# Kernel tuning notes

Hardware: AMD Instinct MI355X
Metric: run time of the kernel (lower is better)

## Reference

```python
import jax, jax.numpy as jnp
import numpy as np

IN_F = 3
HID = 256
N_HIDDEN = 4  # number of hidden SineLayers after the first
OUT_F = 3
OMEGA_0 = 30.0
OMEGA_H = 30.0
N_PTS = 262144


def _uniform(key, shape, bound):
    return jax.random.uniform(key, shape, jnp.float32, -bound, bound)


def setup_inputs() -> dict:
    key = jax.random.key(0)
    ks = jax.random.split(key, 8)
    # coordinates in [-1, 1]
    x = jax.random.uniform(ks[0], (N_PTS, IN_F), jnp.float32, -1.0, 1.0)
    # first layer: W ~ U(-1/n, 1/n)
    w_first = _uniform(ks[1], (HID, IN_F), 1.0 / IN_F)
    b_first = _uniform(ks[2], (HID,), 1.0 / np.sqrt(IN_F))
    # hidden layers: W ~ U(-sqrt(6/n)/omega, sqrt(6/n)/omega), stacked for scan
    hb = np.sqrt(6.0 / HID) / OMEGA_H
    w_hidden = _uniform(ks[3], (N_HIDDEN, HID, HID), hb)
    b_hidden = _uniform(ks[4], (N_HIDDEN, HID), 1.0 / np.sqrt(HID))
    # final linear: same SIREN bound with omega=30
    fb = np.sqrt(6.0 / HID) / 30.0
    w_final = _uniform(ks[5], (OUT_F, HID), fb)
    b_final = _uniform(ks[6], (OUT_F,), 1.0 / np.sqrt(HID))
    return {
        "x": x,
        "w_first": w_first,
        "b_first": b_first,
        "w_hidden": w_hidden,
        "b_hidden": b_hidden,
        "w_final": w_final,
        "b_final": b_final,
    }


def reference(x, w_first, b_first, w_hidden, b_hidden, w_final, b_final):
    # first sine layer: sin(omega_0 * (x W^T + b))
    h = jnp.sin(OMEGA_0 * (x @ w_first.T + b_first))

    # hidden sine layers via scan over stacked [L, HID, HID] weights
    def step(h, wb):
        w, b = wb
        return jnp.sin(OMEGA_H * (h @ w.T + b)), None

    h, _ = jax.lax.scan(step, h, (w_hidden, b_hidden))
    # final linear (no activation: final_activation=None)
    return h @ w_final.T + b_final
```

## Files before the change

### kernel.cpp

```cpp
#include <hip/hip_runtime.h>


typedef _Float16 hf8 __attribute__((ext_vector_type(8)));
typedef _Float16 hf4 __attribute__((ext_vector_type(4)));
typedef float floatx4 __attribute__((ext_vector_type(4)));
typedef unsigned short u16;

#define HID 256
#define NHID 4
#define BM 64
#define THREADS 512
#define NP (BM/16)
#define C_REV 4.774648292756860f
#define WH_ELEMS (NHID*HID*HID)
#define WS_HALVES (WH_ELEMS + 3*HID)

__device__ __forceinline__ float sin_rev(float r){
  float rr = r - rintf(r);
  float s;
  asm("v_sin_f32 %0, %1" : "=v"(s) : "v"(rr));
  return s;
}
__device__ __forceinline__ hf8 ld8h_f32(const float* f){
  const floatx4 a = *(const floatx4*)f;
  const floatx4 b = *(const floatx4*)(f + 4);
  hf8 o;
#pragma unroll
  for (int e = 0; e < 4; ++e){ o[e] = (_Float16)a[e]; o[4+e] = (_Float16)b[e]; }
  return o;
}
__device__ __forceinline__ int hoff(int r, int c){
  return r*HID + (c ^ ((r & 7) << 3));
}

__global__ void prep_kernel(const float* __restrict__ wh,
                            const float* __restrict__ wfin,
                            _Float16* __restrict__ ws){
  const int i = blockIdx.x*256 + threadIdx.x;
  if (i < WH_ELEMS)            ws[i] = (_Float16)wh[i];
  else if (i < WS_HALVES)      ws[i] = (_Float16)wfin[i - WH_ELEMS];
}

template<bool WS>
__global__ __launch_bounds__(THREADS, 4) void siren_kernel(
    const float* __restrict__ x, const float* __restrict__ w_first,
    const float* __restrict__ b_first, const float* __restrict__ w_hidden,
    const float* __restrict__ b_hidden, const float* __restrict__ w_final,
    const float* __restrict__ b_final, const _Float16* __restrict__ wsh,
    float* __restrict__ out)
{
  __shared__ __align__(16) _Float16 hbuf[2][BM*HID];
  __shared__ __align__(16) float    wf[HID*4];
  __shared__ __align__(16) _Float16 wfin[3*HID];

  const int tid = threadIdx.x;
  const int blk = blockIdx.x;

  if (tid < HID){
    wf[tid*4+0] = w_first[tid*3+0] * C_REV;
    wf[tid*4+1] = w_first[tid*3+1] * C_REV;
    wf[tid*4+2] = w_first[tid*3+2] * C_REV;
    wf[tid*4+3] = b_first[tid]     * C_REV;
  } else {
    const int i0 = (tid - HID) * 3;
#pragma unroll
    for (int j = 0; j < 3; ++j){
      const int i = i0 + j;
      if (i < 3*HID) wfin[i] = WS ? wsh[WH_ELEMS + i] : (_Float16)w_final[i];
    }
  }
  __syncthreads();

  {
    const int row = tid & (BM-1);
    const int cb  = (tid >> 6) * 32;
    const int gr  = blk*BM + row;
    const float x0 = x[gr*3+0];
    const float x1 = x[gr*3+1];
    const float x2 = x[gr*3+2];
#pragma unroll
    for (int g = 0; g < 4; ++g){
      hf8 hv;
#pragma unroll
      for (int e = 0; e < 8; ++e){
        const int j = cb + g*8 + e;
        const floatx4 w = *(const floatx4*)(&wf[j*4]);
        float r = w[3];
        r = fmaf(x0, w[0], r);
        r = fmaf(x1, w[1], r);
        r = fmaf(x2, w[2], r);
        hv[e] = (_Float16)sin_rev(r);
      }
      *(hf8*)(&hbuf[0][hoff(row, cb + g*8)]) = hv;
    }
  }
  __syncthreads();

  const int wv  = tid >> 6;
  const int l   = tid & 63;
  const int l15 = l & 15;
  const int l4  = l >> 4;

  const _Float16* rb = &hbuf[0][0];
  _Float16*       wb = &hbuf[1][0];
  for (int L = 0; L < NHID; ++L){
    hf8   wfr[2][8];
    float bC[2][4];
#pragma unroll
    for (int m2 = 0; m2 < 2; ++m2){
      const int jrow  = wv*32 + m2*16 + l15;
      const int wbase = L*HID*HID + jrow*HID + l4*8;
#pragma unroll
      for (int k = 0; k < 8; ++k){
        if (WS) wfr[m2][k] = *(const hf8*)(wsh + wbase + k*32);
        else    wfr[m2][k] = ld8h_f32(w_hidden + wbase + k*32);
      }
      const int j0 = wv*32 + m2*16 + l4*4;
#pragma unroll
      for (int g = 0; g < 4; ++g)
        bC[m2][g] = b_hidden[L*HID + j0 + g] * C_REV;
    }

#pragma unroll
    for (int np = 0; np < NP; ++np){
      const int r = np*16 + l15;
      hf8 bh[8];
#pragma unroll
      for (int k = 0; k < 8; ++k)
        bh[k] = *(const hf8*)(rb + hoff(r, k*32 + l4*8));
      floatx4 acc0 = {0.f,0.f,0.f,0.f};
      floatx4 acc1 = {0.f,0.f,0.f,0.f};
#pragma unroll
      for (int k = 0; k < 8; ++k){
        acc0 = __builtin_amdgcn_mfma_f32_16x16x32_f16(wfr[0][k], bh[k], acc0, 0, 0, 0);
        acc1 = __builtin_amdgcn_mfma_f32_16x16x32_f16(wfr[1][k], bh[k], acc1, 0, 0, 0);
      }
#pragma unroll
      for (int m2 = 0; m2 < 2; ++m2){
        const floatx4 z = m2 ? acc1 : acc0;
        hf4 hv;
#pragma unroll
        for (int g = 0; g < 4; ++g)
          hv[g] = (_Float16)sin_rev(fmaf(z[g], C_REV, bC[m2][g]));
        const int jb = wv*32 + m2*16 + l4*4;
        *(hf4*)(wb + hoff(r, jb)) = hv;
      }
    }
    _Float16* t = (_Float16*)rb; rb = wb; wb = t;
    __syncthreads();
  }

  {
    const int row = tid >> 3;
    const int q   = tid & 7;
    float s0 = 0.f, s1 = 0.f, s2 = 0.f;
#pragma unroll
    for (int i = 0; i < 4; ++i){
      const int c = q*32 + i*8;
      const hf8 hv = *(const hf8*)(rb + hoff(row, c));
      const hf8 w0 = *(const hf8*)(&wfin[0*HID + c]);
      const hf8 w1 = *(const hf8*)(&wfin[1*HID + c]);
      const hf8 w2 = *(const hf8*)(&wfin[2*HID + c]);
#pragma unroll
      for (int e = 0; e < 8; ++e){
        const float h = (float)hv[e];
        s0 = fmaf(h, (float)w0[e], s0);
        s1 = fmaf(h, (float)w1[e], s1);
        s2 = fmaf(h, (float)w2[e], s2);
      }
    }
    s0 += __shfl_xor(s0, 1); s0 += __shfl_xor(s0, 2); s0 += __shfl_xor(s0, 4);
    s1 += __shfl_xor(s1, 1); s1 += __shfl_xor(s1, 2); s1 += __shfl_xor(s1, 4);
    s2 += __shfl_xor(s2, 1); s2 += __shfl_xor(s2, 2); s2 += __shfl_xor(s2, 4);
    if (q == 0){
      const int gr = blk*BM + row;
      out[gr*3+0] = s0 + b_final[0];
      out[gr*3+1] = s1 + b_final[1];
      out[gr*3+2] = s2 + b_final[2];
    }
  }
}

extern "C" void kernel_launch(void* const* d_in, const int* in_sizes, int n_in,
                              void* d_out, int out_size, void* d_ws, size_t ws_size,
                              hipStream_t stream) {
  const float* x        = (const float*)d_in[0];
  const float* w_first  = (const float*)d_in[1];
  const float* b_first  = (const float*)d_in[2];
  const float* w_hidden = (const float*)d_in[3];
  const float* b_hidden = (const float*)d_in[4];
  const float* w_final  = (const float*)d_in[5];
  const float* b_final  = (const float*)d_in[6];
  float* out = (float*)d_out;
  _Float16* wsh = (_Float16*)d_ws;

  const int npts = in_sizes[0] / 3;
  const int grid = npts / BM;
  const bool use_ws = (ws_size >= (size_t)WS_HALVES * sizeof(_Float16));

  if (use_ws){
    const int pgrid = (WS_HALVES + 255) / 256;
    hipLaunchKernelGGL(prep_kernel, dim3(pgrid), dim3(256), 0, stream,
                       w_hidden, w_final, wsh);
    hipLaunchKernelGGL(siren_kernel<true>, dim3(grid), dim3(THREADS), 0, stream,
                       x, w_first, b_first, w_hidden, b_hidden, w_final, b_final,
                       wsh, out);
  } else {
    hipLaunchKernelGGL(siren_kernel<false>, dim3(grid), dim3(THREADS), 0, stream,
                       x, w_first, b_first, w_hidden, b_hidden, w_final, b_final,
                       wsh, out);
  }
}
```

Before: 293.4 us.

## Halve rows per block, raise occupancy, use fract and packed fp16 conversion

Cuts the row tile from 64 to 32 points per block, which halves the shared-memory activation buffers, and raises the launch-bounds occupancy hint from 4 to 8 blocks. Sine range reduction now uses v_fract_f32 instead of subtracting rintf, and fp16 conversion uses packed cvt_pkrtz (round toward zero). Final-layer weights are read directly from global memory instead of being staged in LDS. The risk is that every block still reloads the full hidden weight set into registers, so weight traffic per point doubles, and the tighter register budget may cause spills.

New measurement: 487.0 us. +66.0%, slower.

```diff
diff --git a/kernel.cpp b/kernel.cpp
--- a/kernel.cpp
+++ b/kernel.cpp
@@ -3,12 +3,13 @@
 
 typedef _Float16 hf8 __attribute__((ext_vector_type(8)));
 typedef _Float16 hf4 __attribute__((ext_vector_type(4)));
+typedef _Float16 hf2 __attribute__((ext_vector_type(2)));
+typedef __fp16   fp16x2 __attribute__((ext_vector_type(2)));
 typedef float floatx4 __attribute__((ext_vector_type(4)));
-typedef unsigned short u16;
 
 #define HID 256
 #define NHID 4
-#define BM 64
+#define BM 32
 #define THREADS 512
 #define NP (BM/16)
 #define C_REV 4.774648292756860f
@@ -16,10 +17,14 @@
 #define WS_HALVES (WH_ELEMS + 3*HID)
 
 __device__ __forceinline__ float sin_rev(float r){
-  float rr = r - rintf(r);
-  float s;
-  asm("v_sin_f32 %0, %1" : "=v"(s) : "v"(rr));
+  float f, s;
+  asm("v_fract_f32 %0, %1" : "=v"(f) : "v"(r));
+  asm("v_sin_f32 %0, %1"   : "=v"(s) : "v"(f));
   return s;
+}
+__device__ __forceinline__ hf2 pk2(float a, float b){
+  const fp16x2 p = __builtin_amdgcn_cvt_pkrtz(a, b);
+  return __builtin_bit_cast(hf2, p);
 }
 __device__ __forceinline__ hf8 ld8h_f32(const float* f){
   const floatx4 a = *(const floatx4*)f;
@@ -42,7 +47,7 @@
 }
 
 template<bool WS>
-__global__ __launch_bounds__(THREADS, 4) void siren_kernel(
+__global__ __launch_bounds__(THREADS, 8) void siren_kernel(
     const float* __restrict__ x, const float* __restrict__ w_first,
     const float* __restrict__ b_first, const float* __restrict__ w_hidden,
     const float* __restrict__ b_hidden, const float* __restrict__ w_final,
@@ -51,7 +56,6 @@
 {
   __shared__ __align__(16) _Float16 hbuf[2][BM*HID];
   __shared__ __align__(16) float    wf[HID*4];
-  __shared__ __align__(16) _Float16 wfin[3*HID];
 
   const int tid = threadIdx.x;
   const int blk = blockIdx.x;
@@ -61,26 +65,19 @@
     wf[tid*4+1] = w_first[tid*3+1] * C_REV;
     wf[tid*4+2] = w_first[tid*3+2] * C_REV;
     wf[tid*4+3] = b_first[tid]     * C_REV;
-  } else {
-    const int i0 = (tid - HID) * 3;
-#pragma unroll
-    for (int j = 0; j < 3; ++j){
-      const int i = i0 + j;
-      if (i < 3*HID) wfin[i] = WS ? wsh[WH_ELEMS + i] : (_Float16)w_final[i];
-    }
   }
   __syncthreads();
 
   {
     const int row = tid & (BM-1);
-    const int cb  = (tid >> 6) * 32;
+    const int cb  = (tid >> 5) * 16;
     const int gr  = blk*BM + row;
     const float x0 = x[gr*3+0];
     const float x1 = x[gr*3+1];
     const float x2 = x[gr*3+2];
 #pragma unroll
-    for (int g = 0; g < 4; ++g){
-      hf8 hv;
+    for (int g = 0; g < 2; ++g){
+      float sv[8];
 #pragma unroll
       for (int e = 0; e < 8; ++e){
         const int j = cb + g*8 + e;
@@ -89,7 +86,13 @@
         r = fmaf(x0, w[0], r);
         r = fmaf(x1, w[1], r);
         r = fmaf(x2, w[2], r);
-        hv[e] = (_Float16)sin_rev(r);
+        sv[e] = sin_rev(r);
+      }
+      hf8 hv;
+#pragma unroll
+      for (int p = 0; p < 4; ++p){
+        const hf2 pk = pk2(sv[2*p], sv[2*p+1]);
+        hv[2*p] = pk[0]; hv[2*p+1] = pk[1];
       }
       *(hf8*)(&hbuf[0][hoff(row, cb + g*8)]) = hv;
     }
@@ -138,10 +141,13 @@
 #pragma unroll
       for (int m2 = 0; m2 < 2; ++m2){
         const floatx4 z = m2 ? acc1 : acc0;
-        hf4 hv;
+        float sv[4];
 #pragma unroll
         for (int g = 0; g < 4; ++g)
-          hv[g] = (_Float16)sin_rev(fmaf(z[g], C_REV, bC[m2][g]));
+          sv[g] = sin_rev(fmaf(z[g], C_REV, bC[m2][g]));
+        const hf2 p0 = pk2(sv[0], sv[1]);
+        const hf2 p1 = pk2(sv[2], sv[3]);
+        hf4 hv; hv[0]=p0[0]; hv[1]=p0[1]; hv[2]=p1[0]; hv[3]=p1[1];
         const int jb = wv*32 + m2*16 + l4*4;
         *(hf4*)(wb + hoff(r, jb)) = hv;
       }
@@ -151,16 +157,24 @@
   }
 
   {
-    const int row = tid >> 3;
-    const int q   = tid & 7;
+    const int row = tid >> 4;
+    const int q   = tid & 15;
     float s0 = 0.f, s1 = 0.f, s2 = 0.f;
 #pragma unroll
-    for (int i = 0; i < 4; ++i){
-      const int c = q*32 + i*8;
+    for (int i = 0; i < 2; ++i){
+      const int c = q*16 + i*8;
       const hf8 hv = *(const hf8*)(rb + hoff(row, c));
-      const hf8 w0 = *(const hf8*)(&wfin[0*HID + c]);
-      const hf8 w1 = *(const hf8*)(&wfin[1*HID + c]);
-      const hf8 w2 = *(const hf8*)(&wfin[2*HID + c]);
+      hf8 w0, w1, w2;
+      if (WS){
+        const _Float16* wfh = wsh + WH_ELEMS;
+        w0 = *(const hf8*)(wfh + 0*HID + c);
+        w1 = *(const hf8*)(wfh + 1*HID + c);
+        w2 = *(const hf8*)(wfh + 2*HID + c);
+      } else {
+        w0 = ld8h_f32(w_final + 0*HID + c);
+        w1 = ld8h_f32(w_final + 1*HID + c);
+        w2 = ld8h_f32(w_final + 2*HID + c);
+      }
 #pragma unroll
       for (int e = 0; e < 8; ++e){
         const float h = (float)hv[e];
@@ -169,9 +183,12 @@
         s2 = fmaf(h, (float)w2[e], s2);
       }
     }
-    s0 += __shfl_xor(s0, 1); s0 += __shfl_xor(s0, 2); s0 += __shfl_xor(s0, 4);
-    s1 += __shfl_xor(s1, 1); s1 += __shfl_xor(s1, 2); s1 += __shfl_xor(s1, 4);
-    s2 += __shfl_xor(s2, 1); s2 += __shfl_xor(s2, 2); s2 += __shfl_xor(s2, 4);
+#pragma unroll
+    for (int d = 1; d < 16; d <<= 1){
+      s0 += __shfl_xor(s0, d);
+      s1 += __shfl_xor(s1, d);
+      s2 += __shfl_xor(s2, d);
+    }
     if (q == 0){
       const int gr = blk*BM + row;
       out[gr*3+0] = s0 + b_final[0];
```
